# Kernel optimization log

Measured on AMD Instinct MI355X. Metric: run time of the kernel, lower is better.

The kernel has to match this reference:

```python
import jax, jax.numpy as jnp
import numpy as np

N_DOF = 7
WIDTH = 1024
BATCH = 8192
EPS = 1e-5
LSIZE = N_DOF * (N_DOF + 1) // 2   # diag (n) + strictly-lower ((n^2-n)/2)


def _tri_idx(n):
    # order matches LowTri: offset -i chunks, within-chunk j -> entry (j+i, j)
    r, c = [], []
    for i in range(n):
        for j in range(n - i):
            r.append(j + i)
            c.append(j)
    return np.array(r, np.int32), np.array(c, np.int32)

_R, _C = _tri_idx(N_DOF)


def setup_inputs() -> dict:
    key = jax.random.key(0)
    ks = jax.random.split(key, 9)

    def glorot(k, shape):
        std = (2.0 / (shape[0] + shape[1])) ** 0.5
        return (jax.random.normal(k, shape, jnp.float32) * std).astype(jnp.float32)

    lower = LSIZE - N_DOF
    b0 = 0.1
    return {
        "state": jax.random.normal(ks[0], (BATCH, N_DOF), jnp.float32),
        "velocity": jax.random.normal(ks[1], (BATCH, N_DOF), jnp.float32),
        "acceleration": jax.random.normal(ks[2], (BATCH, N_DOF), jnp.float32),
        "W_in": glorot(ks[3], (N_DOF, WIDTH)), "b_in": jnp.full((WIDTH,), b0, jnp.float32),
        "W_h": glorot(ks[4], (WIDTH, WIDTH)), "b_h": jnp.full((WIDTH,), b0, jnp.float32),
        "W_g": glorot(ks[5], (WIDTH, 1)), "b_g": jnp.full((1,), b0, jnp.float32),
        "W_ld": glorot(ks[6], (WIDTH, N_DOF)), "b_ld": jnp.full((N_DOF,), b0, jnp.float32),
        "W_lo": glorot(ks[7], (WIDTH, lower)), "b_lo": jnp.full((lower,), b0, jnp.float32),
    }


def _layer(x, der, W, b, act):
    # a: [B, out]; der: [B, in, n_dof] -> [B, out, n_dof]
    a = x @ W + b
    if act == "relu":
        y = jax.nn.relu(a)
        gp = (a > 0).astype(a.dtype)
    else:  # linear
        y = a
        gp = jnp.ones_like(a)
    # diag(g'(a)) @ W^T @ prev_der  ==  g'(a)[:, :, None] * (W^T @ prev_der)
    new_der = gp[:, :, None] * jnp.einsum("io,bid->bod", W, der)
    return y, new_der


def _forward(state, velocity, acceleration,
             W_in, b_in, W_h, b_h, W_g, b_g, W_ld, b_ld, W_lo, b_lo):
    B = state.shape[0]
    eye = jnp.broadcast_to(jnp.eye(N_DOF, dtype=state.dtype), (B, N_DOF, N_DOF))

    y1, d1 = _layer(state, eye, W_in, b_in, "relu")
    y2, d2 = _layer(y1, d1, W_h, b_h, "relu")
    y3, d3 = _layer(y2, d2, W_h, b_h, "relu")   # original reuses hidden_layer1 twice

    V, derV = _layer(y3, d3, W_g, b_g, "linear")       # derV: [B, 1, n_dof]
    l_diag, der_ld = _layer(y3, d3, W_ld, b_ld, "relu")
    l_low, der_lo = _layer(y3, d3, W_lo, b_lo, "linear")

    l = jnp.concatenate([l_diag, l_low], axis=1)          # [B, LSIZE]
    der_l = jnp.concatenate([der_ld, der_lo], axis=1)     # [B, LSIZE, n_dof]

    def lowtri(v):   # [B, LSIZE] -> [B, n, n]
        return jnp.zeros((B, N_DOF, N_DOF), v.dtype).at[:, _R, _C].set(v)

    def lowtri3d(v):  # [B, n_dof, LSIZE] -> [B, n_dof, n, n]
        return jnp.zeros((B, N_DOF, N_DOF, N_DOF), v.dtype).at[:, :, _R, _C].set(v)

    L = lowtri(l)
    LT = jnp.swapaxes(L, 1, 2)
    M = L @ LT + EPS * jnp.eye(N_DOF, dtype=L.dtype)

    dldt = jnp.einsum("bld,bd->bl", der_l, velocity)
    dLdt = lowtri(dldt)
    dMdt = L @ jnp.swapaxes(dLdt, 1, 2) + dLdt @ LT

    dLdq = lowtri3d(jnp.swapaxes(der_l, 1, 2))            # [B, n_dof, n, n]
    dMdq = dLdq @ LT[:, None] + L[:, None] @ jnp.swapaxes(dLdq, 2, 3)

    dMdt_dq = jnp.einsum("bij,bj->bi", dMdt, velocity)
    quad_dq = jnp.einsum("bi,bkij,bj->bk", velocity, dMdq, velocity)
    C = dMdt_dq - 0.5 * quad_dq
    G = derV[:, 0, :]                                      # squeeze [B,1,n_dof]
    Mddq = jnp.einsum("bij,bj->bi", M, acceleration)
    tau_pred = Mddq + C + G
    return tau_pred, M, C, G


def reference(state, velocity, acceleration,
              W_in, b_in, W_h, b_h, W_g, b_g, W_ld, b_ld, W_lo, b_lo):
    return _forward(state, velocity, acceleration,
                    W_in, b_in, W_h, b_h, W_g, b_g, W_ld, b_ld, W_lo, b_lo)
```

## Files before the change

### kernel.cpp

```cpp
#include <hip/hip_runtime.h>
#include <hip/hip_bf16.h>
#include <hip/hip_fp16.h>

#define WIDTH 1024
#define BATCH 8192

typedef __attribute__((ext_vector_type(8))) short short8;
typedef __attribute__((ext_vector_type(8))) _Float16 half8;
typedef __attribute__((ext_vector_type(4))) float floatx4;

typedef __attribute__((address_space(1))) void gvoid;
typedef __attribute__((address_space(3))) void lvoid;

__device__ __forceinline__ void async_copy16(const void* g, void* l) {
    __builtin_amdgcn_global_load_lds((gvoid*)g, (lvoid*)l, 16, 0, 0);
}

__device__ __forceinline__ void split_store(float v, __hip_bfloat16* hi, __hip_bfloat16* lo, long idx) {
    __hip_bfloat16 h = __float2bfloat16(v);
    hi[idx] = h;
    lo[idx] = __float2bfloat16(v - __bfloat162float(h));
}

__device__ __forceinline__ floatx4 mfma16(short8 a, short8 b, floatx4 c) {
    return __builtin_amdgcn_mfma_f32_16x16x32_f16(
        __builtin_bit_cast(half8, a), __builtin_bit_cast(half8, b), c, 0, 0, 0);
}
__device__ __forceinline__ floatx4 mfmabf(short8 a, short8 b, floatx4 c) {
    return __builtin_amdgcn_mfma_f32_16x16x32_bf16(a, b, c, 0, 0, 0);
}

template<int N> __device__ __forceinline__ void waitv() {
    if constexpr (N == 0)      asm volatile("s_waitcnt vmcnt(0)" ::: "memory");
    else if constexpr (N == 2) asm volatile("s_waitcnt vmcnt(2)" ::: "memory");
    else if constexpr (N == 4) asm volatile("s_waitcnt vmcnt(4)" ::: "memory");
    else if constexpr (N == 6) asm volatile("s_waitcnt vmcnt(6)" ::: "memory");
    else if constexpr (N == 8) asm volatile("s_waitcnt vmcnt(8)" ::: "memory");
}

__device__ __forceinline__ int swz_col(int s) {
    return ((s & 3) ^ ((s >> 3) & 3)) << 3;
}

__global__ __launch_bounds__(256) void transpose_k(
    const float* __restrict__ W,
    __hip_bfloat16* __restrict__ Wthb, __hip_bfloat16* __restrict__ Wtlb,
    __half* __restrict__ Wtf)
{
    __shared__ float t[32][33];
    const int tx = threadIdx.x & 31, ty = threadIdx.x >> 5;
    const int bx = blockIdx.x << 5, by = blockIdx.y << 5;
#pragma unroll
    for (int r = 0; r < 32; r += 8)
        t[ty + r][tx] = W[(long)(by + ty + r) * WIDTH + bx + tx];
    __syncthreads();
#pragma unroll
    for (int r = 0; r < 32; r += 8) {
        const float v = t[tx][ty + r];
        const long idx = (long)(bx + ty + r) * WIDTH + by + tx;
        split_store(v, Wthb, Wtlb, idx);
        Wtf[idx] = __float2half(v);
    }
}

__global__ __launch_bounds__(256) void buildwcat_k(
    const float* __restrict__ W_ld, const float* __restrict__ W_lo,
    const float* __restrict__ W_g,
    __hip_bfloat16* __restrict__ Wchb, __hip_bfloat16* __restrict__ Wclb,
    __half* __restrict__ Wcf)
{
    const int idx = blockIdx.x * 256 + threadIdx.x;
    const int n = idx >> 10, k = idx & 1023;
    float v = 0.f;
    if (n < 7)       v = W_ld[k * 7 + n];
    else if (n < 28) v = W_lo[k * 21 + (n - 7)];
    else if (n == 28) v = W_g[k];
    split_store(v, Wchb, Wclb, idx);
    Wcf[idx] = __float2half(v);
}

__global__ __launch_bounds__(256) void prep_k(
    const float* __restrict__ state,
    const float* __restrict__ W_in,
    const float* __restrict__ b_in,
    __hip_bfloat16* __restrict__ Y1h, __hip_bfloat16* __restrict__ Y1l,
    __half* __restrict__ D1f)
{
    const int b = blockIdx.x;
    const int j0 = threadIdx.x * 4;
    float s[7];
#pragma unroll
    for (int d = 0; d < 7; ++d) s[d] = state[b * 7 + d];
    float a[4];
#pragma unroll
    for (int q = 0; q < 4; ++q) a[q] = b_in[j0 + q];
    float w[7][4];
#pragma unroll
    for (int d = 0; d < 7; ++d)
#pragma unroll
        for (int q = 0; q < 4; ++q) {
            w[d][q] = W_in[d * WIDTH + j0 + q];
            a[q] += s[d] * w[d][q];
        }
    bool gp[4];
#pragma unroll
    for (int q = 0; q < 4; ++q) {
        gp[q] = a[q] > 0.f;
        split_store(gp[q] ? a[q] : 0.f, Y1h, Y1l, (long)b * WIDTH + j0 + q);
    }
    union { unsigned long long u64; unsigned short h[4]; } pk;
#pragma unroll
    for (int d = 0; d < 7; ++d) {
#pragma unroll
        for (int q = 0; q < 4; ++q) {
            __half v = __float2half(gp[q] ? w[d][q] : 0.f);
            pk.h[q] = *reinterpret_cast<unsigned short*>(&v);
        }
        *reinterpret_cast<unsigned long long*>(&D1f[((long)b * 7 + d) * WIDTH + j0]) = pk.u64;
    }
}

__device__ __forceinline__ void stage_s(
    short* SMbase, const short* __restrict__ src, int tau, int reg, int tid)
{
    short* region = SMbase + ((tau & 1) << 15) + (reg << 13);
    const int wvb = tid & 0x1C0;
    const int kt = tau << 5;
#pragma unroll
    for (int j = 0; j < 2; ++j) {
        const int idx = tid + (j << 9);
        async_copy16(src + (long)(idx >> 2) * WIDTH + kt + swz_col(idx),
                     region + ((long)(wvb + (j << 9)) << 3));
    }
}

template<int W0, int W1, int W2, int IS>
__device__ __forceinline__ void ys_step(
    short* SM, const short* pAh, const short* pAl, const short* pBh, const short* pBl,
    int t, int tid, int wm, int wn, int r, int kqs, floatx4 (&acc)[8][4])
{
    short* buf = SM + ((t & 1) << 15);
    short8 ah[8], bh[4];
#pragma unroll
    for (int i = 0; i < 8; ++i)
        ah[i] = *reinterpret_cast<const short8*>(&buf[(wm * 128 + i * 16 + r) * 32 + kqs]);
#pragma unroll
    for (int j = 0; j < 4; ++j)
        bh[j] = *reinterpret_cast<const short8*>(&buf[8192 + (wn * 64 + j * 16 + r) * 32 + kqs]);
    if (IS) { stage_s(SM, pAh, t + 1, 0, tid); stage_s(SM, pBh, t + 1, 1, tid); }
    __builtin_amdgcn_s_barrier();
    asm volatile("s_waitcnt lgkmcnt(0)");
    __builtin_amdgcn_sched_barrier(0);
    __builtin_amdgcn_s_setprio(1);
#pragma unroll
    for (int i = 0; i < 8; ++i)
#pragma unroll
        for (int j = 0; j < 4; ++j)
            acc[i][j] = mfmabf(ah[i], bh[j], acc[i][j]);
    __builtin_amdgcn_s_setprio(0);
    waitv<W0>();
    __builtin_amdgcn_s_barrier();
    short8 al[8];
#pragma unroll
    for (int i = 0; i < 8; ++i)
        al[i] = *reinterpret_cast<const short8*>(&buf[16384 + (wm * 128 + i * 16 + r) * 32 + kqs]);
    if (IS) stage_s(SM, pAl, t + 1, 2, tid);
    __builtin_amdgcn_s_barrier();
    asm volatile("s_waitcnt lgkmcnt(0)");
    __builtin_amdgcn_sched_barrier(0);
    __builtin_amdgcn_s_setprio(1);
#pragma unroll
    for (int i = 0; i < 8; ++i)
#pragma unroll
        for (int j = 0; j < 4; ++j)
            acc[i][j] = mfmabf(al[i], bh[j], acc[i][j]);
    __builtin_amdgcn_s_setprio(0);
    waitv<W1>();
    __builtin_amdgcn_s_barrier();
    short8 bl[4];
#pragma unroll
    for (int j = 0; j < 4; ++j)
        bl[j] = *reinterpret_cast<const short8*>(&buf[24576 + (wn * 64 + j * 16 + r) * 32 + kqs]);
    if (IS) stage_s(SM, pBl, t + 1, 3, tid);
    __builtin_amdgcn_s_barrier();
    asm volatile("s_waitcnt lgkmcnt(0)");
    __builtin_amdgcn_sched_barrier(0);
    __builtin_amdgcn_s_setprio(1);
#pragma unroll
    for (int i = 0; i < 8; ++i)
#pragma unroll
        for (int j = 0; j < 4; ++j)
            acc[i][j] = mfmabf(ah[i], bl[j], acc[i][j]);
    __builtin_amdgcn_s_setprio(0);
    waitv<W2>();
    __builtin_amdgcn_s_barrier();
}

__device__ __forceinline__ void ys_gemm_256(
    short* SM, const short* Ah, const short* Al, const short* Bh, const short* Bl,
    int tid, int wm, int wn, int r, int kqs, floatx4 (&acc)[8][4])
{
    stage_s(SM, Ah, 0, 0, tid);
    stage_s(SM, Bh, 0, 1, tid);
    stage_s(SM, Al, 0, 2, tid);
    stage_s(SM, Bl, 0, 3, tid);
    waitv<4>();
    __builtin_amdgcn_s_barrier();
#pragma unroll 2
    for (int t = 0; t < 31; ++t)
        ys_step<6, 6, 4, 1>(SM, Ah, Al, Bh, Bl, t, tid, wm, wn, r, kqs, acc);
    ys_step<2, 0, 99, 0>(SM, Ah, Al, Bh, Bl, 31, tid, wm, wn, r, kqs, acc);
}

__device__ __forceinline__ void stage_chunk_d2(
    short* SMbase, const short* __restrict__ A, const short* __restrict__ B,
    int tau, int c, int tid)
{
    const short* src = (c & 1) ? B : A;
    const int kbase = (tau << 6) + ((c >> 1) << 5);
    short* region = SMbase + ((tau & 1) << 15) + (c << 13);
    const int wvb = tid & 0x1C0;
#pragma unroll
    for (int j = 0; j < 2; ++j) {
        const int idx = tid + (j << 9);
        async_copy16(src + (long)(idx >> 2) * WIDTH + kbase + swz_col(idx),
                     region + ((long)(wvb + (j << 9)) << 3));
    }
}

__device__ __forceinline__ void d_gemm_256(
    short* SM, const short* Abase, const short* Bbase, int tid,
    int wm, int wn, int r, int kqs, floatx4 (&acc)[8][4])
{
    stage_chunk_d2(SM, Abase, Bbase, 0, 0, tid);
    stage_chunk_d2(SM, Abase, Bbase, 0, 1, tid);
    stage_chunk_d2(SM, Abase, Bbase, 0, 2, tid);
    stage_chunk_d2(SM, Abase, Bbase, 0, 3, tid);
    stage_chunk_d2(SM, Abase, Bbase, 1, 0, tid);
    stage_chunk_d2(SM, Abase, Bbase, 1, 1, tid);
    waitv<8>();
    __builtin_amdgcn_s_barrier();

    short8 af[8], bf[4];
#pragma unroll 2
    for (int t = 0; t < 16; ++t) {
        short* buf = SM + ((t & 1) << 15);
#pragma unroll
        for (int ks = 0; ks < 2; ++ks) {
            const short* Ab = buf + (ks ? 2 : 0) * 8192;
            const short* Bb = buf + (ks ? 3 : 1) * 8192;

#pragma unroll
            for (int i = 0; i < 4; ++i)
                af[i] = *reinterpret_cast<const short8*>(&Ab[(wm * 128 + i * 16 + r) * 32 + kqs]);
#pragma unroll
            for (int j = 0; j < 4; ++j)
                bf[j] = *reinterpret_cast<const short8*>(&Bb[(wn * 64 + j * 16 + r) * 32 + kqs]);
            if (ks == 0) { if (t + 1 < 16) stage_chunk_d2(SM, Abase, Bbase, t + 1, 2, tid); }
            else         { if (t + 2 < 16) stage_chunk_d2(SM, Abase, Bbase, t + 2, 0, tid); }
            __builtin_amdgcn_s_barrier();
            asm volatile("s_waitcnt lgkmcnt(0)");
            __builtin_amdgcn_sched_barrier(0);
            __builtin_amdgcn_s_setprio(1);
#pragma unroll
            for (int i = 0; i < 4; ++i)
#pragma unroll
                for (int j = 0; j < 4; ++j)
                    acc[i][j] = mfma16(af[i], bf[j], acc[i][j]);
            __builtin_amdgcn_s_setprio(0);
            __builtin_amdgcn_s_barrier();

#pragma unroll
            for (int i = 0; i < 4; ++i)
                af[4 + i] = *reinterpret_cast<const short8*>(&Ab[(wm * 128 + (4 + i) * 16 + r) * 32 + kqs]);
            if (ks == 0) { if (t + 1 < 16) stage_chunk_d2(SM, Abase, Bbase, t + 1, 3, tid); }
            else         { if (t + 2 < 16) stage_chunk_d2(SM, Abase, Bbase, t + 2, 1, tid); }
            __builtin_amdgcn_s_barrier();
            asm volatile("s_waitcnt lgkmcnt(0)");
            __builtin_amdgcn_sched_barrier(0);
            __builtin_amdgcn_s_setprio(1);
#pragma unroll
            for (int i = 0; i < 4; ++i)
#pragma unroll
                for (int j = 0; j < 4; ++j)
                    acc[4 + i][j] = mfma16(af[4 + i], bf[j], acc[4 + i][j]);
            __builtin_amdgcn_s_setprio(0);
            if (ks == 0) {
                if (t < 15) waitv<8>(); else waitv<0>();
            } else {
                if (t < 14) waitv<8>(); else if (t == 14) waitv<4>();
            }
            __builtin_amdgcn_s_barrier();
        }
    }
}

__device__ __forceinline__ void y_epilogue_s(
    floatx4 (&acc)[8][4], const float* __restrict__ bias,
    __hip_bfloat16* __restrict__ outh, __hip_bfloat16* __restrict__ outl,
    int bx, int by, int wm, int wn, int r, int r4)
{
#pragma unroll
    for (int i = 0; i < 8; ++i)
#pragma unroll
        for (int j = 0; j < 4; ++j) {
            const int col = by * 256 + wn * 64 + j * 16 + r;
#pragma unroll
            for (int rr = 0; rr < 4; ++rr) {
                const int row = bx * 256 + wm * 128 + i * 16 + r4 + rr;
                float v = acc[i][j][rr] + bias[col];
                v = v > 0.f ? v : 0.f;
                split_store(v, outh, outl, (long)row * WIDTH + col);
            }
        }
}

__global__ __launch_bounds__(512, 2) void gemm_ys(
    const __hip_bfloat16* __restrict__ Ah, const __hip_bfloat16* __restrict__ Al,
    const __hip_bfloat16* __restrict__ Bh, const __hip_bfloat16* __restrict__ Bl,
    const float* __restrict__ bias,
    __hip_bfloat16* __restrict__ outh, __hip_bfloat16* __restrict__ outl)
{
    __shared__ __align__(16) short SM[65536];
    const int tid = threadIdx.x;
    const int lane = tid & 63, wv = tid >> 6;
    const int wm = wv >> 2, wn = wv & 3;
    const int r = lane & 15, r4 = (lane >> 4) << 2;
    const int kqs = (((lane >> 4) ^ ((r >> 1) & 3)) << 3);
    const int bm = blockIdx.x >> 2, bn = blockIdx.x & 3;
    floatx4 acc[8][4] = {};
    ys_gemm_256(SM, (const short*)Ah + (long)bm * 256 * WIDTH,
                (const short*)Al + (long)bm * 256 * WIDTH,
                (const short*)Bh + (long)bn * 256 * WIDTH,
                (const short*)Bl + (long)bn * 256 * WIDTH, tid, wm, wn, r, kqs, acc);
    y_epilogue_s(acc, bias, outh, outl, bm, bn, wm, wn, r, r4);
}

__global__ __launch_bounds__(512, 2) void d2y3_8p(
    const __half* __restrict__ D1,
    const __half* __restrict__ Wtf,
    const __hip_bfloat16* __restrict__ Wthb, const __hip_bfloat16* __restrict__ Wtlb,
    const __hip_bfloat16* __restrict__ Y2h, const __hip_bfloat16* __restrict__ Y2l,
    const float* __restrict__ bias,
    __half* __restrict__ D2out,
    __hip_bfloat16* __restrict__ Y3h, __hip_bfloat16* __restrict__ Y3l,
    int ny)
{
    __shared__ __align__(16) short SM[65536];
    const int tid = threadIdx.x;
    const int lane = tid & 63, wv = tid >> 6;
    const int wm = wv >> 2, wn = wv & 3;
    const int r = lane & 15, r4 = (lane >> 4) << 2;
    const int kqs = (((lane >> 4) ^ ((r >> 1) & 3)) << 3);

    floatx4 acc[8][4] = {};
    if ((int)blockIdx.x < ny * 4) {
        const int bm = blockIdx.x >> 2, bn = blockIdx.x & 3;
        ys_gemm_256(SM, (const short*)Y2h + (long)bm * 256 * WIDTH,
                    (const short*)Y2l + (long)bm * 256 * WIDTH,
                    (const short*)Wthb + (long)bn * 256 * WIDTH,
                    (const short*)Wtlb + (long)bn * 256 * WIDTH, tid, wm, wn, r, kqs, acc);
        y_epilogue_s(acc, bias, Y3h, Y3l, bm, bn, wm, wn, r, r4);
        return;
    }

    const int d = blockIdx.x - ny * 4;
    const int bm = d >> 2, bn = d & 3;
    d_gemm_256(SM, (const short*)D1 + (long)bm * 256 * WIDTH,
               (const short*)Wtf + (long)bn * 256 * WIDTH, tid, wm, wn, r, kqs, acc);

#pragma unroll
    for (int i = 0; i < 8; ++i)
#pragma unroll
        for (int j = 0; j < 4; ++j) {
            const int col = bn * 256 + wn * 64 + j * 16 + r;
#pragma unroll
            for (int rr = 0; rr < 4; ++rr) {
                const int row = bm * 256 + wm * 128 + i * 16 + r4 + rr;
                float v = acc[i][j][rr];
                const unsigned brow = (unsigned)row / 7u;
                if (!(__bfloat162float(Y2h[(long)brow * WIDTH + col]) > 0.f)) v = 0.f;
                D2out[(long)row * WIDTH + col] = __float2half(v);
            }
        }
}

__device__ __forceinline__ void heady_half(
    short* SMh, int bm, int tl,
    const __hip_bfloat16* __restrict__ Y3h, const __hip_bfloat16* __restrict__ Y3l,
    const __hip_bfloat16* __restrict__ Wch, const __hip_bfloat16* __restrict__ Wcl,
    float* __restrict__ PY)
{
    short* Ash = SMh;          short* Asl = SMh + 4096;
    short* Bsh = SMh + 8192;   short* Bsl = SMh + 9216;
    const int lane = tl & 63;
    const int wv = tl >> 6;
    const int r = lane & 15, r4 = (lane >> 4) << 2;
    const int kqs = (((lane >> 4) ^ ((r >> 1) & 3)) << 3);
    const int srow = tl >> 2, scol = (tl & 3) << 3;
    const int swc = (((tl & 3) ^ ((srow >> 1) & 3)) << 3);
    const long half = 64l * WIDTH;
    const short* pAh = (const short*)Y3h + (long)(bm * 128 + srow) * WIDTH + swc;
    const short* pAl = (const short*)Y3l + (long)(bm * 128 + srow) * WIDTH + swc;
    const long boff = (long)srow * WIDTH + scol;
    const short* pBh = (const short*)Wch;  const short* pBl = (const short*)Wcl;

    floatx4 acc[2][2] = {};
    for (int kt = 0; kt < WIDTH; kt += 32) {
        short8 gbh, gbl;
        if (tl < 128) {
            gbh = *reinterpret_cast<const short8*>(pBh + boff + kt);
            gbl = *reinterpret_cast<const short8*>(pBl + boff + kt);
        }
        __syncthreads();
        async_copy16(pAh + kt,        Ash + wv * 512);
        async_copy16(pAh + half + kt, Ash + 2048 + wv * 512);
        async_copy16(pAl + kt,        Asl + wv * 512);
        async_copy16(pAl + half + kt, Asl + 2048 + wv * 512);
        if (tl < 128) {
            *reinterpret_cast<short8*>(&Bsh[srow * 32 + swc]) = gbh;
            *reinterpret_cast<short8*>(&Bsl[srow * 32 + swc]) = gbl;
        }
        __syncthreads();
        short8 afh[2], afl[2], bfh[2], bfl[2];
#pragma unroll
        for (int i = 0; i < 2; ++i) {
            const int ar = (wv * 32 + i * 16 + r) * 32 + kqs;
            afh[i] = *reinterpret_cast<const short8*>(&Ash[ar]);
            afl[i] = *reinterpret_cast<const short8*>(&Asl[ar]);
        }
#pragma unroll
        for (int j = 0; j < 2; ++j) {
            const int br = (j * 16 + r) * 32 + kqs;
            bfh[j] = *reinterpret_cast<const short8*>(&Bsh[br]);
            bfl[j] = *reinterpret_cast<const short8*>(&Bsl[br]);
        }
#pragma unroll
        for (int i = 0; i < 2; ++i)
#pragma unroll
            for (int j = 0; j < 2; ++j) {
                acc[i][j] = mfmabf(afh[i], bfh[j], acc[i][j]);
                acc[i][j] = mfmabf(afh[i], bfl[j], acc[i][j]);
                acc[i][j] = mfmabf(afl[i], bfh[j], acc[i][j]);
            }
    }
#pragma unroll
    for (int i = 0; i < 2; ++i)
#pragma unroll
        for (int j = 0; j < 2; ++j)
#pragma unroll
            for (int rr = 0; rr < 4; ++rr) {
                const int row = bm * 128 + wv * 32 + i * 16 + r4 + rr;
                PY[(long)row * 32 + j * 16 + r] = acc[i][j][rr];
            }
}

__global__ __launch_bounds__(512, 2) void d3pd_8p(
    const __half* __restrict__ D2,
    const __half* __restrict__ Wtf,
    const __hip_bfloat16* __restrict__ Y3h, const __hip_bfloat16* __restrict__ Y3l,
    const __half* __restrict__ Wcf,
    const __hip_bfloat16* __restrict__ Wchb, const __hip_bfloat16* __restrict__ Wclb,
    float* __restrict__ PDpart, float* __restrict__ PY,
    int nd2, int Mrows)
{
    __shared__ __align__(16) short SM[65536];
    const int tid = threadIdx.x;

    if ((int)blockIdx.x >= nd2 * 4) {
        const int hd = (blockIdx.x - nd2 * 4) * 2 + (tid >> 8);
        heady_half(SM + (tid >> 8) * 10240, hd, tid & 255, Y3h, Y3l, Wchb, Wclb, PY);
        return;
    }

    const int lane = tid & 63, wv = tid >> 6;
    const int wm = wv >> 2, wn = wv & 3;
    const int r = lane & 15, kq = (lane >> 4) << 3, r4 = (lane >> 4) << 2;
    const int kqs = (((lane >> 4) ^ ((r >> 1) & 3)) << 3);
    const int bm = blockIdx.x >> 2, bn = blockIdx.x & 3;

    floatx4 acc[8][4] = {};
    d_gemm_256(SM, (const short*)D2 + (long)bm * 256 * WIDTH,
               (const short*)Wtf + (long)bn * 256 * WIDTH, tid, wm, wn, r, kqs, acc);

    short* T   = SM;
    short* WcH = SM + 34816;

    floatx4 accp[2][2] = {};
#pragma unroll
    for (int h = 0; h < 2; ++h) {
        __syncthreads();
        if ((wn >> 1) == h) {
#pragma unroll
            for (int i = 0; i < 8; ++i)
#pragma unroll
                for (int j = 0; j < 4; ++j) {
                    const int ct = (wn & 1) * 64 + j * 16 + r;
                    const int colg = bn * 256 + h * 128 + ct;
#pragma unroll
                    for (int rr = 0; rr < 4; ++rr) {
                        const int rowl = wm * 128 + i * 16 + r4 + rr;
                        const int rowg = bm * 256 + rowl;
                        float v = acc[i][j][rr];
                        const unsigned brow = (unsigned)rowg / 7u;
                        if (!(__bfloat162float(Y3h[(long)brow * WIDTH + colg]) > 0.f)) v = 0.f;
                        __half hb = __float2half(v);
                        T[rowl * 136 + ct] = *reinterpret_cast<short*>(&hb);
                    }
                }
        }
        {
            const int n = tid >> 4, k8 = (tid & 15) * 8;
            const short* wh = (const short*)Wcf;
            *reinterpret_cast<short8*>(&WcH[n * 136 + k8]) =
                *reinterpret_cast<const short8*>(wh + (long)n * WIDTH + bn * 256 + h * 128 + k8);
        }
        __syncthreads();
#pragma unroll
        for (int kk = 0; kk < 128; kk += 32) {
            short8 af2[2], bh8[2];
#pragma unroll
            for (int i = 0; i < 2; ++i)
                af2[i] = *reinterpret_cast<const short8*>(&T[(wv * 32 + i * 16 + r) * 136 + kk + kq]);
#pragma unroll
            for (int j = 0; j < 2; ++j)
                bh8[j] = *reinterpret_cast<const short8*>(&WcH[(j * 16 + r) * 136 + kk + kq]);
#pragma unroll
            for (int i = 0; i < 2; ++i)
#pragma unroll
                for (int j = 0; j < 2; ++j)
                    accp[i][j] = mfma16(af2[i], bh8[j], accp[i][j]);
        }
    }
#pragma unroll
    for (int i = 0; i < 2; ++i)
#pragma unroll
        for (int j = 0; j < 2; ++j)
#pragma unroll
            for (int rr = 0; rr < 4; ++rr) {
                const int rowg = bm * 256 + wv * 32 + i * 16 + r4 + rr;
                PDpart[((long)bn * Mrows + rowg) * 32 + j * 16 + r] = accp[i][j][rr];
            }
}

__device__ __forceinline__ int midx(int rr, int cc) {
    const int i = rr - cc;
    return i * 7 - (i * (i - 1)) / 2 + cc;
}

__global__ __launch_bounds__(64) void finalize_k(
    const float* __restrict__ PY,
    const float* __restrict__ PDpart,
    const float* __restrict__ vel_g,
    const float* __restrict__ acc_g,
    const float* __restrict__ b_ld,
    const float* __restrict__ b_lo,
    float* __restrict__ out,
    int b0, int Mrows)
{
    __shared__ float lval[28];
    __shared__ int gpv[7];
    __shared__ float derl[29 * 7];
    __shared__ float Lm[49], Mm[49], dLt[49], uu[49];
    __shared__ float wvv[7], pv[7], Cv[7], Gv[7], tauv[7], vl[7], ac[7];

    const int bl = blockIdx.x, tid = threadIdx.x;
    const int b = b0 + bl;
    if (tid < 28) {
        float s = PY[(long)bl * 32 + tid];
        if (tid < 7) {
            s += b_ld[tid];
            gpv[tid] = s > 0.f;
            lval[tid] = s > 0.f ? s : 0.f;
        } else {
            lval[tid] = s + b_lo[tid - 7];
        }
    }
    if (tid >= 28 && tid < 35) {
        vl[tid - 28] = vel_g[b * 7 + tid - 28];
        ac[tid - 28] = acc_g[b * 7 + tid - 28];
    }
    __syncthreads();
    for (int idx = tid; idx < 203; idx += 64) {
        const int m = idx / 7, d = idx % 7;
        float v = 0.f;
#pragma unroll
        for (int p = 0; p < 4; ++p)
            v += PDpart[((long)p * Mrows + bl * 7 + d) * 32 + m];
        if (m < 7 && !gpv[m]) v = 0.f;
        derl[m * 7 + d] = v;
    }
    __syncthreads();
    if (tid < 49) {
        const int rr = tid / 7, cc = tid % 7;
        Lm[tid] = (rr >= cc) ? lval[midx(rr, cc)] : 0.f;
    }
    __syncthreads();
    if (tid < 49) {
        const int rr = tid / 7, cc = tid % 7;
        float s = 0.f;
        for (int k = 0; k < 7; ++k) s += Lm[rr * 7 + k] * Lm[cc * 7 + k];
        if (rr == cc) s += 1e-5f;
        Mm[tid] = s;
        float t = 0.f;
        if (rr >= cc) {
            const int m = midx(rr, cc);
            for (int d = 0; d < 7; ++d) t += derl[m * 7 + d] * vl[d];
        }
        dLt[tid] = t;
        float u = 0.f;
        for (int r2 = cc; r2 < 7; ++r2) u += vl[r2] * derl[midx(r2, cc) * 7 + rr];
        uu[tid] = u;
    } else if (tid >= 49 && tid < 56) {
        const int j = tid - 49;
        float s = 0.f;
        for (int r2 = 0; r2 < 7; ++r2) s += Lm[r2 * 7 + j] * vl[r2];
        wvv[j] = s;
    }
    __syncthreads();
    if (tid < 7) {
        float s = 0.f;
        for (int r2 = 0; r2 < 7; ++r2) s += dLt[r2 * 7 + tid] * vl[r2];
        pv[tid] = s;
    }
    __syncthreads();
    if (tid < 7) {
        float s = 0.f, q = 0.f, md = 0.f;
        for (int c = 0; c < 7; ++c) {
            s += Lm[tid * 7 + c] * pv[c] + dLt[tid * 7 + c] * wvv[c];
            q += uu[tid * 7 + c] * wvv[c];
            md += Mm[tid * 7 + c] * ac[c];
        }
        Cv[tid] = s - q;
        Gv[tid] = derl[28 * 7 + tid];
        tauv[tid] = md + Cv[tid] + Gv[tid];
    }
    __syncthreads();
    if (tid < 49) out[57344 + (long)b * 49 + tid] = Mm[tid];
    if (tid < 7) {
        out[(long)b * 7 + tid] = tauv[tid];
        out[458752 + (long)b * 7 + tid] = Cv[tid];
        out[516096 + (long)b * 7 + tid] = Gv[tid];
    }
}

extern "C" void kernel_launch(void* const* d_in, const int* in_sizes, int n_in,
                              void* d_out, int out_size, void* d_ws, size_t ws_size,
                              hipStream_t stream)
{
    const float* state = (const float*)d_in[0];
    const float* vel   = (const float*)d_in[1];
    const float* accel = (const float*)d_in[2];
    const float* W_in  = (const float*)d_in[3];
    const float* b_in  = (const float*)d_in[4];
    const float* W_h   = (const float*)d_in[5];
    const float* b_h   = (const float*)d_in[6];
    const float* W_g   = (const float*)d_in[7];
    const float* W_ld  = (const float*)d_in[9];
    const float* b_ld  = (const float*)d_in[10];
    const float* W_lo  = (const float*)d_in[11];
    const float* b_lo  = (const float*)d_in[12];
    float* outp = (float*)d_out;

    char* ws = (char*)d_ws;
    __hip_bfloat16* Wthb = (__hip_bfloat16*)ws; ws += (size_t)WIDTH * WIDTH * 2;
    __hip_bfloat16* Wtlb = (__hip_bfloat16*)ws; ws += (size_t)WIDTH * WIDTH * 2;
    __half*         Wtf  = (__half*)ws;         ws += (size_t)WIDTH * WIDTH * 2;
    __hip_bfloat16* Wchb = (__hip_bfloat16*)ws; ws += 32 * WIDTH * 2;
    __hip_bfloat16* Wclb = (__hip_bfloat16*)ws; ws += 32 * WIDTH * 2;
    __half*         Wcf  = (__half*)ws;         ws += 32 * WIDTH * 2;
    const size_t fixed = (size_t)(ws - (char*)d_ws);

    int CH = 256;
    for (int cand = 8192; cand >= 256; cand >>= 1) {
        size_t need = fixed + (size_t)cand * 36992;
        if (need <= ws_size) { CH = cand; break; }
    }
    const int NCH = BATCH / CH;

    const size_t YB = (size_t)CH * WIDTH * 2;
    const size_t DB = (size_t)CH * 7 * WIDTH * 2;
    __hip_bfloat16* Yah = (__hip_bfloat16*)ws; ws += YB;
    __hip_bfloat16* Yal = (__hip_bfloat16*)ws; ws += YB;
    __hip_bfloat16* Ybh = (__hip_bfloat16*)ws; ws += YB;
    __hip_bfloat16* Ybl = (__hip_bfloat16*)ws; ws += YB;
    __half* Daf = (__half*)ws; ws += DB;
    __half* Dbf = (__half*)ws; ws += DB;
    float* PY = (float*)ws; ws += (size_t)CH * 32 * 4;
    float* PDpart = (float*)Daf;

    const int Mrows = CH * 7;
    const int nd2 = Mrows / 256;
    const int ny256 = CH / 256;

    transpose_k<<<dim3(32, 32), dim3(256), 0, stream>>>(W_h, Wthb, Wtlb, Wtf);
    buildwcat_k<<<dim3(128), dim3(256), 0, stream>>>(W_ld, W_lo, W_g, Wchb, Wclb, Wcf);

    for (int c = 0; c < NCH; ++c) {
        prep_k<<<dim3(CH), dim3(256), 0, stream>>>(state + (size_t)c * CH * 7, W_in, b_in,
                                                   Yah, Yal, Daf);
        gemm_ys<<<dim3(ny256 * 4), dim3(512), 0, stream>>>(
            Yah, Yal, Wthb, Wtlb, b_h, Ybh, Ybl);
        d2y3_8p<<<dim3((ny256 + nd2) * 4), dim3(512), 0, stream>>>(
            Daf, Wtf, Wthb, Wtlb, Ybh, Ybl, b_h, Dbf, Yah, Yal, ny256);
        d3pd_8p<<<dim3(nd2 * 4 + ny256), dim3(512), 0, stream>>>(
            Dbf, Wtf, Yah, Yal, Wcf, Wchb, Wclb, PDpart, PY, nd2, Mrows);
        finalize_k<<<dim3(CH), dim3(64), 0, stream>>>(PY, PDpart, vel, accel, b_ld, b_lo,
                                                      outp, c * CH, Mrows);
    }
    (void)in_sizes; (void)n_in; (void)out_size;
}
```

Baseline: 656.9 us.

## Use 128x256 split-bf16 Y GEMM tiles with deeper prefetch and XCD-aware block mapping

Replaces the 256x256 split-bf16 hidden-layer GEMM with a 128x256 tile that uses 4x4 accumulators per wave and a two-step-ahead prefetch of the hi/lo operand chunks into double-buffered LDS. The smaller tile doubles the number of Y blocks, which should improve CU occupancy and load balance. A new xcd_map remaps block indices so that neighbouring row tiles land on the same XCD and share L2. The trade-off is less A/B reuse per block and more finely tuned vmcnt waits, which must match the number of loads in flight exactly.

```diff
diff --git a/kernel.cpp b/kernel.cpp
--- a/kernel.cpp
+++ b/kernel.cpp
@@ -32,14 +32,27 @@
 
 template<int N> __device__ __forceinline__ void waitv() {
     if constexpr (N == 0)      asm volatile("s_waitcnt vmcnt(0)" ::: "memory");
-    else if constexpr (N == 2) asm volatile("s_waitcnt vmcnt(2)" ::: "memory");
+    else if constexpr (N == 1) asm volatile("s_waitcnt vmcnt(1)" ::: "memory");
+    else if constexpr (N == 3) asm volatile("s_waitcnt vmcnt(3)" ::: "memory");
     else if constexpr (N == 4) asm volatile("s_waitcnt vmcnt(4)" ::: "memory");
     else if constexpr (N == 6) asm volatile("s_waitcnt vmcnt(6)" ::: "memory");
+    else if constexpr (N == 7) asm volatile("s_waitcnt vmcnt(7)" ::: "memory");
     else if constexpr (N == 8) asm volatile("s_waitcnt vmcnt(8)" ::: "memory");
+    else if constexpr (N == 9) asm volatile("s_waitcnt vmcnt(9)" ::: "memory");
 }
 
 __device__ __forceinline__ int swz_col(int s) {
     return ((s & 3) ^ ((s >> 3) & 3)) << 3;
+}
+
+__device__ __forceinline__ void xcd_map(int idx, int nm, int& bm, int& bn) {
+    if ((nm & 7) == 0) {
+        bm = (idx & 7) | ((idx >> 5) << 3);
+        bn = (idx >> 3) & 3;
+    } else {
+        bm = idx >> 2;
+        bn = idx & 3;
+    }
 }
 
 __global__ __launch_bounds__(256) void transpose_k(
@@ -120,96 +133,144 @@
     }
 }
 
-__device__ __forceinline__ void stage_s(
-    short* SMbase, const short* __restrict__ src, int tau, int reg, int tid)
-{
-    short* region = SMbase + ((tau & 1) << 15) + (reg << 13);
-    const int wvb = tid & 0x1C0;
-    const int kt = tau << 5;
+
+__device__ __forceinline__ void st128(const short* src, short* region, int tid, int kbase) {
+    async_copy16(src + (long)(tid >> 2) * WIDTH + kbase + swz_col(tid),
+                 region + ((tid & 0x1C0) << 3));
+}
+__device__ __forceinline__ void st256(const short* src, short* region, int tid, int kbase) {
 #pragma unroll
     for (int j = 0; j < 2; ++j) {
         const int idx = tid + (j << 9);
-        async_copy16(src + (long)(idx >> 2) * WIDTH + kt + swz_col(idx),
-                     region + ((long)(wvb + (j << 9)) << 3));
+        async_copy16(src + (long)(idx >> 2) * WIDTH + kbase + swz_col(idx),
+                     region + (((tid & 0x1C0) + (j << 9)) << 3));
     }
 }
 
 template<int W0, int W1, int W2, int IS>
-__device__ __forceinline__ void ys_step(
-    short* SM, const short* pAh, const short* pAl, const short* pBh, const short* pBl,
-    int t, int tid, int wm, int wn, int r, int kqs, floatx4 (&acc)[8][4])
-{
-    short* buf = SM + ((t & 1) << 15);
-    short8 ah[8], bh[4];
-#pragma unroll
-    for (int i = 0; i < 8; ++i)
-        ah[i] = *reinterpret_cast<const short8*>(&buf[(wm * 128 + i * 16 + r) * 32 + kqs]);
+__device__ __forceinline__ void y8_triple(
+    short* buf, short* nbuf,
+    const short* pAh, const short* pAl, const short* pBh, const short* pBl,
+    int t, int tid, int wm, int wn, int r, int kqs, floatx4 (&acc)[4][4])
+{
+    short8 fah[4], fbh[4];
+#pragma unroll
+    for (int i = 0; i < 4; ++i)
+        fah[i] = *reinterpret_cast<const short8*>(&buf[(wm * 64 + i * 16 + r) * 32 + kqs]);
 #pragma unroll
     for (int j = 0; j < 4; ++j)
-        bh[j] = *reinterpret_cast<const short8*>(&buf[8192 + (wn * 64 + j * 16 + r) * 32 + kqs]);
-    if (IS) { stage_s(SM, pAh, t + 1, 0, tid); stage_s(SM, pBh, t + 1, 1, tid); }
+        fbh[j] = *reinterpret_cast<const short8*>(&buf[8192 + (wn * 64 + j * 16 + r) * 32 + kqs]);
+    if (IS >= 1) st128(pAl, nbuf + 4096, tid, (t + 1) * 32);
     __builtin_amdgcn_s_barrier();
     asm volatile("s_waitcnt lgkmcnt(0)");
     __builtin_amdgcn_sched_barrier(0);
     __builtin_amdgcn_s_setprio(1);
 #pragma unroll
-    for (int i = 0; i < 8; ++i)
+    for (int i = 0; i < 4; ++i)
 #pragma unroll
         for (int j = 0; j < 4; ++j)
-            acc[i][j] = mfmabf(ah[i], bh[j], acc[i][j]);
+            acc[i][j] = mfmabf(fah[i], fbh[j], acc[i][j]);
     __builtin_amdgcn_s_setprio(0);
     waitv<W0>();
     __builtin_amdgcn_s_barrier();
-    short8 al[8];
-#pragma unroll
-    for (int i = 0; i < 8; ++i)
-        al[i] = *reinterpret_cast<const short8*>(&buf[16384 + (wm * 128 + i * 16 + r) * 32 + kqs]);
-    if (IS) stage_s(SM, pAl, t + 1, 2, tid);
+    short8 fbl[4];
+#pragma unroll
+    for (int j = 0; j < 4; ++j)
+        fbl[j] = *reinterpret_cast<const short8*>(&buf[16384 + (wn * 64 + j * 16 + r) * 32 + kqs]);
+    if (IS >= 2) { st128(pAh, buf, tid, (t + 2) * 32); st256(pBh, buf + 8192, tid, (t + 2) * 32); }
     __builtin_amdgcn_s_barrier();
     asm volatile("s_waitcnt lgkmcnt(0)");
     __builtin_amdgcn_sched_barrier(0);
     __builtin_amdgcn_s_setprio(1);
 #pragma unroll
-    for (int i = 0; i < 8; ++i)
+    for (int i = 0; i < 4; ++i)
 #pragma unroll
         for (int j = 0; j < 4; ++j)
-            acc[i][j] = mfmabf(al[i], bh[j], acc[i][j]);
+            acc[i][j] = mfmabf(fah[i], fbl[j], acc[i][j]);
     __builtin_amdgcn_s_setprio(0);
     waitv<W1>();
     __builtin_amdgcn_s_barrier();
-    short8 bl[4];
-#pragma unroll
-    for (int j = 0; j < 4; ++j)
-        bl[j] = *reinterpret_cast<const short8*>(&buf[24576 + (wn * 64 + j * 16 + r) * 32 + kqs]);
-    if (IS) stage_s(SM, pBl, t + 1, 3, tid);
+    short8 fal[4];
+#pragma unroll
+    for (int i = 0; i < 4; ++i)
+        fal[i] = *reinterpret_cast<const short8*>(&buf[4096 + (wm * 64 + i * 16 + r) * 32 + kqs]);
+    if (IS >= 2) st256(pBl, buf + 16384, tid, (t + 2) * 32);
     __builtin_amdgcn_s_barrier();
     asm volatile("s_waitcnt lgkmcnt(0)");
     __builtin_amdgcn_sched_barrier(0);
     __builtin_amdgcn_s_setprio(1);
 #pragma unroll
-    for (int i = 0; i < 8; ++i)
+    for (int i = 0; i < 4; ++i)
 #pragma unroll
         for (int j = 0; j < 4; ++j)
-            acc[i][j] = mfmabf(ah[i], bl[j], acc[i][j]);
+            acc[i][j] = mfmabf(fal[i], fbh[j], acc[i][j]);
     __builtin_amdgcn_s_setprio(0);
     waitv<W2>();
     __builtin_amdgcn_s_barrier();
 }
 
-__device__ __forceinline__ void ys_gemm_256(
-    short* SM, const short* Ah, const short* Al, const short* Bh, const short* Bl,
-    int tid, int wm, int wn, int r, int kqs, floatx4 (&acc)[8][4])
-{
-    stage_s(SM, Ah, 0, 0, tid);
-    stage_s(SM, Bh, 0, 1, tid);
-    stage_s(SM, Al, 0, 2, tid);
-    stage_s(SM, Bl, 0, 3, tid);
-    waitv<4>();
+__device__ __forceinline__ void y8_gemm_body(
+    short* SM,
+    int bm, int bn, int tid,
+    const __hip_bfloat16* Ah_, const __hip_bfloat16* Al_,
+    const __hip_bfloat16* Bh_, const __hip_bfloat16* Bl_,
+    const float* bias,
+    __hip_bfloat16* outh, __hip_bfloat16* outl)
+{
+    const int lane = tid & 63, wv = tid >> 6;
+    const int wm = wv >> 2, wn = wv & 3;
+    const int r = lane & 15, r4 = (lane >> 4) << 2;
+    const int kqs = (((lane >> 4) ^ ((r >> 1) & 3)) << 3);
+    const short* pAh = (const short*)Ah_ + (long)bm * 128 * WIDTH;
+    const short* pAl = (const short*)Al_ + (long)bm * 128 * WIDTH;
+    const short* pBh = (const short*)Bh_ + (long)bn * 256 * WIDTH;
+    const short* pBl = (const short*)Bl_ + (long)bn * 256 * WIDTH;
+
+    floatx4 acc[4][4] = {};
+
+    st128(pAh, SM + 0,     tid, 0);
+    st256(pBh, SM + 8192,  tid, 0);
+    st256(pBl, SM + 16384, tid, 0);
+    st128(pAl, SM + 4096,  tid, 0);
+    st128(pAh, SM + 24576 + 0,     tid, 32);
+    st256(pBh, SM + 24576 + 8192,  tid, 32);
+    st256(pBl, SM + 24576 + 16384, tid, 32);
+    waitv<8>();
     __builtin_amdgcn_s_barrier();
-#pragma unroll 2
-    for (int t = 0; t < 31; ++t)
-        ys_step<6, 6, 4, 1>(SM, Ah, Al, Bh, Bl, t, tid, wm, wn, r, kqs, acc);
-    ys_step<2, 0, 99, 0>(SM, Ah, Al, Bh, Bl, 31, tid, wm, wn, r, kqs, acc);
+
+    for (int t2 = 0; t2 < 15; ++t2) {
+        y8_triple<7, 9, 8, 2>(SM,         SM + 24576, pAh, pAl, pBh, pBl, 2 * t2,     tid, wm, wn, r, kqs, acc);
+        y8_triple<7, 9, 8, 2>(SM + 24576, SM,         pAh, pAl, pBh, pBl, 2 * t2 + 1, tid, wm, wn, r, kqs, acc);
+    }
+    y8_triple<7, 6, 3, 1>(SM,         SM + 24576, pAh, pAl, pBh, pBl, 30, tid, wm, wn, r, kqs, acc);
+    y8_triple<1, 0, 0, 0>(SM + 24576, SM,         pAh, pAl, pBh, pBl, 31, tid, wm, wn, r, kqs, acc);
+
+#pragma unroll
+    for (int i = 0; i < 4; ++i)
+#pragma unroll
+        for (int j = 0; j < 4; ++j) {
+            const int col = bn * 256 + wn * 64 + j * 16 + r;
+#pragma unroll
+            for (int rr = 0; rr < 4; ++rr) {
+                const int row = bm * 128 + wm * 64 + i * 16 + r4 + rr;
+                float v = acc[i][j][rr] + bias[col];
+                v = v > 0.f ? v : 0.f;
+                split_store(v, outh, outl, (long)row * WIDTH + col);
+            }
+        }
+}
+
+__global__ __launch_bounds__(512, 2) void gemm_y8(
+    const __hip_bfloat16* __restrict__ Ah, const __hip_bfloat16* __restrict__ Al,
+    const __hip_bfloat16* __restrict__ Bh, const __hip_bfloat16* __restrict__ Bl,
+    const float* __restrict__ bias,
+    __hip_bfloat16* __restrict__ outh, __hip_bfloat16* __restrict__ outl,
+    int ny)
+{
+    __shared__ __align__(16) short SM[49152];
+    int bm, bn;
+    xcd_map(blockIdx.x, ny, bm, bn);
+    y8_gemm_body(SM, bm, bn, threadIdx.x, Ah, Al, Bh, Bl, bias, outh, outl);
 }
 
 __device__ __forceinline__ void stage_chunk_d2(
@@ -295,47 +356,6 @@
     }
 }
 
-__device__ __forceinline__ void y_epilogue_s(
-    floatx4 (&acc)[8][4], const float* __restrict__ bias,
-    __hip_bfloat16* __restrict__ outh, __hip_bfloat16* __restrict__ outl,
-    int bx, int by, int wm, int wn, int r, int r4)
-{
-#pragma unroll
-    for (int i = 0; i < 8; ++i)
-#pragma unroll
-        for (int j = 0; j < 4; ++j) {
-            const int col = by * 256 + wn * 64 + j * 16 + r;
-#pragma unroll
-            for (int rr = 0; rr < 4; ++rr) {
-                const int row = bx * 256 + wm * 128 + i * 16 + r4 + rr;
-                float v = acc[i][j][rr] + bias[col];
-                v = v > 0.f ? v : 0.f;
-                split_store(v, outh, outl, (long)row * WIDTH + col);
-            }
-        }
-}
-
-__global__ __launch_bounds__(512, 2) void gemm_ys(
-    const __hip_bfloat16* __restrict__ Ah, const __hip_bfloat16* __restrict__ Al,
-    const __hip_bfloat16* __restrict__ Bh, const __hip_bfloat16* __restrict__ Bl,
-    const float* __restrict__ bias,
-    __hip_bfloat16* __restrict__ outh, __hip_bfloat16* __restrict__ outl)
-{
-    __shared__ __align__(16) short SM[65536];
-    const int tid = threadIdx.x;
-    const int lane = tid & 63, wv = tid >> 6;
-    const int wm = wv >> 2, wn = wv & 3;
-    const int r = lane & 15, r4 = (lane >> 4) << 2;
-    const int kqs = (((lane >> 4) ^ ((r >> 1) & 3)) << 3);
-    const int bm = blockIdx.x >> 2, bn = blockIdx.x & 3;
-    floatx4 acc[8][4] = {};
-    ys_gemm_256(SM, (const short*)Ah + (long)bm * 256 * WIDTH,
-                (const short*)Al + (long)bm * 256 * WIDTH,
-                (const short*)Bh + (long)bn * 256 * WIDTH,
-                (const short*)Bl + (long)bn * 256 * WIDTH, tid, wm, wn, r, kqs, acc);
-    y_epilogue_s(acc, bias, outh, outl, bm, bn, wm, wn, r, r4);
-}
-
 __global__ __launch_bounds__(512, 2) void d2y3_8p(
     const __half* __restrict__ D1,
     const __half* __restrict__ Wtf,
@@ -344,28 +364,27 @@
     const float* __restrict__ bias,
     __half* __restrict__ D2out,
     __hip_bfloat16* __restrict__ Y3h, __hip_bfloat16* __restrict__ Y3l,
-    int ny)
+    int ny128, int nd2)
 {
     __shared__ __align__(16) short SM[65536];
     const int tid = threadIdx.x;
+
+    if ((int)blockIdx.x < ny128 * 4) {
+        int bm, bn;
+        xcd_map(blockIdx.x, ny128, bm, bn);
+        y8_gemm_body(SM, bm, bn, tid, Y2h, Y2l, Wthb, Wtlb, bias, Y3h, Y3l);
+        return;
+    }
+
     const int lane = tid & 63, wv = tid >> 6;
     const int wm = wv >> 2, wn = wv & 3;
     const int r = lane & 15, r4 = (lane >> 4) << 2;
     const int kqs = (((lane >> 4) ^ ((r >> 1) & 3)) << 3);
 
+    int bm, bn;
+    xcd_map(blockIdx.x - ny128 * 4, nd2, bm, bn);
+
     floatx4 acc[8][4] = {};
-    if ((int)blockIdx.x < ny * 4) {
-        const int bm = blockIdx.x >> 2, bn = blockIdx.x & 3;
-        ys_gemm_256(SM, (const short*)Y2h + (long)bm * 256 * WIDTH,
-                    (const short*)Y2l + (long)bm * 256 * WIDTH,
-                    (const short*)Wthb + (long)bn * 256 * WIDTH,
-                    (const short*)Wtlb + (long)bn * 256 * WIDTH, tid, wm, wn, r, kqs, acc);
-        y_epilogue_s(acc, bias, Y3h, Y3l, bm, bn, wm, wn, r, r4);
-        return;
-    }
-
-    const int d = blockIdx.x - ny * 4;
-    const int bm = d >> 2, bn = d & 3;
     d_gemm_256(SM, (const short*)D1 + (long)bm * 256 * WIDTH,
                (const short*)Wtf + (long)bn * 256 * WIDTH, tid, wm, wn, r, kqs, acc);
 
@@ -477,7 +496,8 @@
     const int wm = wv >> 2, wn = wv & 3;
     const int r = lane & 15, kq = (lane >> 4) << 3, r4 = (lane >> 4) << 2;
     const int kqs = (((lane >> 4) ^ ((r >> 1) & 3)) << 3);
-    const int bm = blockIdx.x >> 2, bn = blockIdx.x & 3;
+    int bm, bn;
+    xcd_map(blockIdx.x, nd2, bm, bn);
 
     floatx4 acc[8][4] = {};
     d_gemm_256(SM, (const short*)D2 + (long)bm * 256 * WIDTH,
@@ -691,7 +711,7 @@
 
     const int Mrows = CH * 7;
     const int nd2 = Mrows / 256;
-    const int ny256 = CH / 256;
+    const int ny128 = CH / 128;
 
     transpose_k<<<dim3(32, 32), dim3(256), 0, stream>>>(W_h, Wthb, Wtlb, Wtf);
     buildwcat_k<<<dim3(128), dim3(256), 0, stream>>>(W_ld, W_lo, W_g, Wchb, Wclb, Wcf);
@@ -699,11 +719,11 @@
     for (int c = 0; c < NCH; ++c) {
         prep_k<<<dim3(CH), dim3(256), 0, stream>>>(state + (size_t)c * CH * 7, W_in, b_in,
                                                    Yah, Yal, Daf);
-        gemm_ys<<<dim3(ny256 * 4), dim3(512), 0, stream>>>(
-            Yah, Yal, Wthb, Wtlb, b_h, Ybh, Ybl);
-        d2y3_8p<<<dim3((ny256 + nd2) * 4), dim3(512), 0, stream>>>(
-            Daf, Wtf, Wthb, Wtlb, Ybh, Ybl, b_h, Dbf, Yah, Yal, ny256);
-        d3pd_8p<<<dim3(nd2 * 4 + ny256), dim3(512), 0, stream>>>(
+        gemm_y8<<<dim3(ny128 * 4), dim3(512), 0, stream>>>(
+            Yah, Yal, Wthb, Wtlb, b_h, Ybh, Ybl, ny128);
+        d2y3_8p<<<dim3((ny128 + nd2) * 4), dim3(512), 0, stream>>>(
+            Daf, Wtf, Wthb, Wtlb, Ybh, Ybl, b_h, Dbf, Yah, Yal, ny128, nd2);
+        d3pd_8p<<<dim3(nd2 * 4 + ny128 / 2), dim3(512), 0, stream>>>(
             Dbf, Wtf, Yah, Yal, Wcf, Wchb, Wclb, PDpart, PY, nd2, Mrows);
         finalize_k<<<dim3(CH), dim3(64), 0, stream>>>(PY, PDpart, vel, accel, b_ld, b_lo,
                                                       outp, c * CH, Mrows);
```

Result: faster. 570.6 us (-13.1%).
